# Optimization experiments

Measured on AMD Instinct MI355X. Metric: run time of the kernel, lower is better.

The kernel has to match this reference:

```python
import jax, jax.numpy as jnp
import numpy as np

N_SENT = 65536
N_BAGS = 4096
REL_DIM = 768
FLAT_C = 53
GLOBAL_C = 95


def setup_inputs() -> dict:
    key = jax.random.key(0)
    k1, k2, k3, k4, k5 = jax.random.split(key, 5)
    x = jax.random.normal(k1, (N_SENT, REL_DIM), dtype=jnp.float32)
    attention_query = jax.random.randint(k2, (N_SENT, 3), 0, GLOBAL_C, dtype=jnp.int32)
    # strictly increasing interior boundaries -> every bag non-empty
    rng = np.random.RandomState(0)
    interior = np.sort(rng.choice(np.arange(1, N_SENT), N_BAGS - 1, replace=False))
    scope = jnp.asarray(np.concatenate([[0], interior, [N_SENT]]), dtype=jnp.int32)
    # learned params (xavier-like scale for embeddings, normal bias)
    attention_weight = jax.random.normal(k3, (GLOBAL_C, REL_DIM), dtype=jnp.float32) * (2.0 / (GLOBAL_C + REL_DIM)) ** 0.5
    relation_weight = jax.random.normal(k4, (FLAT_C, REL_DIM * 3), dtype=jnp.float32) * (2.0 / (FLAT_C + REL_DIM * 3)) ** 0.5
    bias = jax.random.normal(k5, (FLAT_C,), dtype=jnp.float32)
    return {"x": x, "attention_query": attention_query, "scope": scope,
            "attention_weight": attention_weight, "relation_weight": relation_weight,
            "bias": bias}


def _segment_ids(scope, n):
    # scope: [B+1] offsets; build per-sentence bag id via boundary scatter + cumsum
    marks = jnp.zeros((n,), dtype=jnp.int32).at[scope[1:-1]].add(1)
    return jnp.cumsum(marks)


def reference(x, attention_query, scope, attention_weight, relation_weight, bias):
    n = x.shape[0]
    n_bags = scope.shape[0] - 1
    seg = _segment_ids(scope, n)  # [N]

    # per-layer attention logits: sum(x * attention_emb, -1) for all 3 layers at once
    att = attention_weight[attention_query]                # [N, 3, D]
    logit = jnp.einsum('nd,nld->nl', x, att)               # [N, 3]

    # segment (per-bag) softmax over sentences, per layer
    seg_max = jax.ops.segment_max(logit, seg, num_segments=n_bags)   # [B, 3]
    w = jnp.exp(logit - seg_max[seg])
    denom = jax.ops.segment_sum(w, seg, num_segments=n_bags)         # [B, 3]
    w = w / denom[seg]                                               # [N, 3]

    # weighted sentence aggregation per bag, per layer
    bag = jax.ops.segment_sum(w[:, :, None] * x[:, None, :], seg, num_segments=n_bags)  # [B, 3, D]

    stack_logits_layers = jnp.transpose(bag, (1, 0, 2))    # [3, B, D]
    logits_total = bag.reshape(n_bags, -1)                 # [B, 3*D] == cat(layer0, layer1, layer2)
    # dropout in eval mode (identity); global_ratio > 0 -> compute probs
    probs = logits_total @ relation_weight.T + bias        # [B, FLAT_C]
    return (stack_logits_layers, logits_total, probs)
```

## Files before the change

### kernel.cpp

```cpp
#include <hip/hip_runtime.h>
#include <math.h>

#define NSENT 65536
#define NBAGS 4096
#define DIM 768
#define D4 192
#define FLATC 53
#define CPAD 64
#define KTOT 2304
#define K4 576
#define CHUNK 256

typedef short bf16x8 __attribute__((ext_vector_type(8)));
typedef float f32x4 __attribute__((ext_vector_type(4)));

__device__ __forceinline__ float wsum(float v) {
#pragma unroll
  for (int o = 32; o; o >>= 1) v += __shfl_xor(v, o);
  return v;
}
__device__ __forceinline__ float wmax(float v) {
#pragma unroll
  for (int o = 32; o; o >>= 1) v = fmaxf(v, __shfl_xor(v, o));
  return v;
}
__device__ __forceinline__ float dot4(float4 a, float4 b) {
  return a.x * b.x + a.y * b.y + a.z * b.z + a.w * b.w;
}
__device__ __forceinline__ unsigned short f2bf(float f) {
  unsigned int u = __float_as_uint(f);
  return (unsigned short)((u + 0x7FFFu + ((u >> 16) & 1u)) >> 16);
}

__global__ __launch_bounds__(192) void bag_kernel(
    const float* __restrict__ x, const int* __restrict__ q,
    const int* __restrict__ scope, const float* __restrict__ aw,
    float* __restrict__ out, unsigned short* __restrict__ lt16) {
  const int b = blockIdx.x;
  const int s0 = scope[b];
  const int s1 = scope[b + 1];
  const int len = s1 - s0;
  const int tid = threadIdx.x;
  const int wave = tid >> 6;
  const int lane = tid & 63;

  __shared__ float lg[CHUNK][3];
  __shared__ int sq[CHUNK][3];
  __shared__ float sm[3], se[3];

  float m[3] = {-INFINITY, -INFINITY, -INFINITY};
  float dsum[3] = {0.f, 0.f, 0.f};
  float4 acc[3];
#pragma unroll
  for (int l = 0; l < 3; l++) acc[l] = make_float4(0.f, 0.f, 0.f, 0.f);

  const float4* __restrict__ X4 = (const float4*)x;
  const float4* __restrict__ AW4 = (const float4*)aw;

  for (int cs = 0; cs < len; cs += CHUNK) {
    const int clen = min(CHUNK, len - cs);

    for (int idx = tid; idx < 3 * clen; idx += 192)
      ((int*)sq)[idx] = q[(size_t)(s0 + cs) * 3 + idx];
    __syncthreads();

    for (int i0 = wave; i0 < clen; i0 += 6) {
      const int i1 = i0 + 3;
      const bool h2 = (i1 < clen);
      const int i1c = h2 ? i1 : i0;
      const int n0 = s0 + cs + i0;
      const int n1 = s0 + cs + i1c;
      const int qa0 = sq[i0][0], qa1 = sq[i0][1], qa2 = sq[i0][2];
      const int qb0 = sq[i1c][0], qb1 = sq[i1c][1], qb2 = sq[i1c][2];
      const float4* xr0 = X4 + (size_t)n0 * D4;
      const float4* xr1 = X4 + (size_t)n1 * D4;
      const float4* A00 = AW4 + (size_t)qa0 * D4;
      const float4* A01 = AW4 + (size_t)qa1 * D4;
      const float4* A02 = AW4 + (size_t)qa2 * D4;
      const float4* A10 = AW4 + (size_t)qb0 * D4;
      const float4* A11 = AW4 + (size_t)qb1 * D4;
      const float4* A12 = AW4 + (size_t)qb2 * D4;
      float p00 = 0.f, p01 = 0.f, p02 = 0.f;
      float p10 = 0.f, p11 = 0.f, p12 = 0.f;
#pragma unroll
      for (int j = 0; j < 3; j++) {
        const int idx = lane + 64 * j;
        const float4 x0 = xr0[idx];
        const float4 x1 = xr1[idx];
        p00 += dot4(x0, A00[idx]);
        p01 += dot4(x0, A01[idx]);
        p02 += dot4(x0, A02[idx]);
        p10 += dot4(x1, A10[idx]);
        p11 += dot4(x1, A11[idx]);
        p12 += dot4(x1, A12[idx]);
      }
      p00 = wsum(p00); p01 = wsum(p01); p02 = wsum(p02);
      p10 = wsum(p10); p11 = wsum(p11); p12 = wsum(p12);
      if (lane == 0) {
        lg[i0][0] = p00; lg[i0][1] = p01; lg[i0][2] = p02;
        if (h2) { lg[i1][0] = p10; lg[i1][1] = p11; lg[i1][2] = p12; }
      }
    }
    __syncthreads();

    {
      const int l = wave;
      float cm = -INFINITY;
      for (int i = lane; i < clen; i += 64) cm = fmaxf(cm, lg[i][l]);
      cm = wmax(cm);
      const float mn = fmaxf(m[l], cm);
      float es = 0.f;
      for (int i = lane; i < clen; i += 64) {
        const float e = __expf(lg[i][l] - mn);
        es += e;
        lg[i][l] = e;
      }
      es = wsum(es);
      if (lane == 0) {
        sm[l] = mn;
        se[l] = es;
      }
    }
    __syncthreads();

#pragma unroll
    for (int l = 0; l < 3; l++) {
      const float mn = sm[l];
      const float sc = __expf(m[l] - mn);
      m[l] = mn;
      dsum[l] = dsum[l] * sc + se[l];
      acc[l].x *= sc; acc[l].y *= sc; acc[l].z *= sc; acc[l].w *= sc;
    }

    {
      int i = 0;
      for (; i + 1 < clen; i += 2) {
        const float w00 = lg[i][0], w01 = lg[i][1], w02 = lg[i][2];
        const float w10 = lg[i + 1][0], w11 = lg[i + 1][1], w12 = lg[i + 1][2];
        const float4 x0 = X4[(size_t)(s0 + cs + i) * D4 + tid];
        const float4 x1 = X4[(size_t)(s0 + cs + i + 1) * D4 + tid];
        acc[0].x += w00 * x0.x + w10 * x1.x;
        acc[0].y += w00 * x0.y + w10 * x1.y;
        acc[0].z += w00 * x0.z + w10 * x1.z;
        acc[0].w += w00 * x0.w + w10 * x1.w;
        acc[1].x += w01 * x0.x + w11 * x1.x;
        acc[1].y += w01 * x0.y + w11 * x1.y;
        acc[1].z += w01 * x0.z + w11 * x1.z;
        acc[1].w += w01 * x0.w + w11 * x1.w;
        acc[2].x += w02 * x0.x + w12 * x1.x;
        acc[2].y += w02 * x0.y + w12 * x1.y;
        acc[2].z += w02 * x0.z + w12 * x1.z;
        acc[2].w += w02 * x0.w + w12 * x1.w;
      }
      if (i < clen) {
        const float w0 = lg[i][0], w1 = lg[i][1], w2 = lg[i][2];
        const float4 xv = X4[(size_t)(s0 + cs + i) * D4 + tid];
        acc[0].x += w0 * xv.x; acc[0].y += w0 * xv.y; acc[0].z += w0 * xv.z; acc[0].w += w0 * xv.w;
        acc[1].x += w1 * xv.x; acc[1].y += w1 * xv.y; acc[1].z += w1 * xv.z; acc[1].w += w1 * xv.w;
        acc[2].x += w2 * xv.x; acc[2].y += w2 * xv.y; acc[2].z += w2 * xv.z; acc[2].w += w2 * xv.w;
      }
    }
    __syncthreads();
  }

  float4* o0 = (float4*)out;
  float4* o1 = (float4*)(out + (size_t)3 * NBAGS * DIM);
  ushort4* l16 = (ushort4*)(lt16 + (size_t)b * KTOT);
#pragma unroll
  for (int l = 0; l < 3; l++) {
    const float inv = (dsum[l] > 0.f) ? (1.f / dsum[l]) : 0.f;
    float4 v = acc[l];
    v.x *= inv; v.y *= inv; v.z *= inv; v.w *= inv;
    o0[((size_t)l * NBAGS + b) * D4 + tid] = v;
    o1[(size_t)b * K4 + l * D4 + tid] = v;
    ushort4 h;
    h.x = f2bf(v.x); h.y = f2bf(v.y); h.z = f2bf(v.z); h.w = f2bf(v.w);
    l16[l * D4 + tid] = h;
  }
}

__global__ __launch_bounds__(256) void rwcvt(const float* __restrict__ rw,
                                             unsigned short* __restrict__ rw16) {
  const int idx = blockIdx.x * 256 + threadIdx.x;
  if (idx < CPAD * KTOT) {
    const int row = idx / KTOT;
    const float v = (row < FLATC) ? rw[idx] : 0.f;
    rw16[idx] = f2bf(v);
  }
}

__global__ __launch_bounds__(256) void probs_mfma(
    const unsigned short* __restrict__ lt16,
    const unsigned short* __restrict__ rw16,
    const float* __restrict__ bias, float* __restrict__ outp) {
  const int wv = threadIdx.x >> 6;
  const int lane = threadIdx.x & 63;
  const int r = lane & 15;
  const int kg = lane >> 4;
  const int bagbase = blockIdx.x * 64 + wv * 16;

  f32x4 acc[4];
#pragma unroll
  for (int ct = 0; ct < 4; ct++) acc[ct] = (f32x4){0.f, 0.f, 0.f, 0.f};

  const unsigned short* ap = lt16 + (size_t)(bagbase + r) * KTOT + kg * 8;
  const unsigned short* bp[4];
#pragma unroll
  for (int ct = 0; ct < 4; ct++)
    bp[ct] = rw16 + (size_t)(ct * 16 + r) * KTOT + kg * 8;

  for (int k = 0; k < KTOT; k += 32) {
    const bf16x8 a = *(const bf16x8*)(ap + k);
#pragma unroll
    for (int ct = 0; ct < 4; ct++) {
      const bf16x8 bb = *(const bf16x8*)(bp[ct] + k);
      acc[ct] = __builtin_amdgcn_mfma_f32_16x16x32_bf16(a, bb, acc[ct], 0, 0, 0);
    }
  }

#pragma unroll
  for (int ct = 0; ct < 4; ct++) {
    const int col = ct * 16 + r;
    if (col < FLATC) {
      const float bv = bias[col];
#pragma unroll
      for (int reg = 0; reg < 4; reg++) {
        const int bag = bagbase + kg * 4 + reg;
        outp[(size_t)bag * FLATC + col] = acc[ct][reg] + bv;
      }
    }
  }
}

extern "C" void kernel_launch(void* const* d_in, const int* in_sizes, int n_in,
                              void* d_out, int out_size, void* d_ws,
                              size_t ws_size, hipStream_t stream) {
  const float* x = (const float*)d_in[0];
  const int* aq = (const int*)d_in[1];
  const int* scope = (const int*)d_in[2];
  const float* aw = (const float*)d_in[3];
  const float* rw = (const float*)d_in[4];
  const float* bias = (const float*)d_in[5];
  float* out = (float*)d_out;

  unsigned short* lt16 = (unsigned short*)d_ws;
  unsigned short* rw16 = lt16 + (size_t)NBAGS * KTOT;

  hipLaunchKernelGGL(bag_kernel, dim3(NBAGS), dim3(192), 0, stream, x, aq,
                     scope, aw, out, lt16);
  hipLaunchKernelGGL(rwcvt, dim3((CPAD * KTOT + 255) / 256), dim3(256), 0,
                     stream, rw, rw16);

  float* probs = out + (size_t)3 * NBAGS * DIM + (size_t)NBAGS * KTOT;
  hipLaunchKernelGGL(probs_mfma, dim3(NBAGS / 64), dim3(256), 0, stream, lt16,
                     rw16, bias, probs);
}
```

Measured before the change: 187.3 us.

## Split logit computation into a separate sentence-parallel kernel before bag aggregation

Moves the per-sentence attention logit dot products out of the per-bag kernel into a standalone kernel that runs two sentences per wave across all sentences, writing logits to a workspace buffer. The bag kernel then only loads precomputed logits, does the segment softmax and the weighted sum. This removes the load imbalance of uneven bag sizes during the logit phase. The trade-off is that x is now read from memory twice, plus an extra launch. The chunk size is doubled and the weighted-sum loop is unrolled by four to put more loads in flight.

```diff
diff --git a/kernel.cpp b/kernel.cpp
--- a/kernel.cpp
+++ b/kernel.cpp
@@ -9,7 +9,7 @@
 #define CPAD 64
 #define KTOT 2304
 #define K4 576
-#define CHUNK 256
+#define CHUNK 512
 
 typedef short bf16x8 __attribute__((ext_vector_type(8)));
 typedef float f32x4 __attribute__((ext_vector_type(4)));
@@ -32,10 +32,59 @@
   return (unsigned short)((u + 0x7FFFu + ((u >> 16) & 1u)) >> 16);
 }
 
-__global__ __launch_bounds__(192) void bag_kernel(
+__global__ __launch_bounds__(256) void logit_kernel(
     const float* __restrict__ x, const int* __restrict__ q,
-    const int* __restrict__ scope, const float* __restrict__ aw,
-    float* __restrict__ out, unsigned short* __restrict__ lt16) {
+    const float* __restrict__ aw, float* __restrict__ lgout) {
+  const int wid = (blockIdx.x * 256 + threadIdx.x) >> 6;
+  const int lane = threadIdx.x & 63;
+  const int n0 = wid * 2;
+  if (n0 >= NSENT) return;
+  const int n1 = n0 + 1;
+
+  const int qa0 = q[3 * n0 + 0], qa1 = q[3 * n0 + 1], qa2 = q[3 * n0 + 2];
+  const int qb0 = q[3 * n1 + 0], qb1 = q[3 * n1 + 1], qb2 = q[3 * n1 + 2];
+
+  const float4* __restrict__ X4 = (const float4*)x;
+  const float4* __restrict__ AW4 = (const float4*)aw;
+  const float4* xr0 = X4 + (size_t)n0 * D4;
+  const float4* xr1 = X4 + (size_t)n1 * D4;
+  const float4* A00 = AW4 + (size_t)qa0 * D4;
+  const float4* A01 = AW4 + (size_t)qa1 * D4;
+  const float4* A02 = AW4 + (size_t)qa2 * D4;
+  const float4* A10 = AW4 + (size_t)qb0 * D4;
+  const float4* A11 = AW4 + (size_t)qb1 * D4;
+  const float4* A12 = AW4 + (size_t)qb2 * D4;
+
+  float p00 = 0.f, p01 = 0.f, p02 = 0.f;
+  float p10 = 0.f, p11 = 0.f, p12 = 0.f;
+#pragma unroll
+  for (int j = 0; j < 3; j++) {
+    const int idx = lane + 64 * j;
+    const float4 x0 = xr0[idx];
+    const float4 x1 = xr1[idx];
+    p00 += dot4(x0, A00[idx]);
+    p01 += dot4(x0, A01[idx]);
+    p02 += dot4(x0, A02[idx]);
+    p10 += dot4(x1, A10[idx]);
+    p11 += dot4(x1, A11[idx]);
+    p12 += dot4(x1, A12[idx]);
+  }
+  p00 = wsum(p00); p01 = wsum(p01); p02 = wsum(p02);
+  p10 = wsum(p10); p11 = wsum(p11); p12 = wsum(p12);
+  if (lane == 0) {
+    lgout[3 * n0 + 0] = p00;
+    lgout[3 * n0 + 1] = p01;
+    lgout[3 * n0 + 2] = p02;
+    lgout[3 * n1 + 0] = p10;
+    lgout[3 * n1 + 1] = p11;
+    lgout[3 * n1 + 2] = p12;
+  }
+}
+
+__global__ __launch_bounds__(192) void bag_sum(
+    const float* __restrict__ x, const float* __restrict__ lgin,
+    const int* __restrict__ scope, float* __restrict__ out,
+    unsigned short* __restrict__ lt16) {
   const int b = blockIdx.x;
   const int s0 = scope[b];
   const int s1 = scope[b + 1];
@@ -45,7 +94,6 @@
   const int lane = tid & 63;
 
   __shared__ float lg[CHUNK][3];
-  __shared__ int sq[CHUNK][3];
   __shared__ float sm[3], se[3];
 
   float m[3] = {-INFINITY, -INFINITY, -INFINITY};
@@ -55,52 +103,12 @@
   for (int l = 0; l < 3; l++) acc[l] = make_float4(0.f, 0.f, 0.f, 0.f);
 
   const float4* __restrict__ X4 = (const float4*)x;
-  const float4* __restrict__ AW4 = (const float4*)aw;
 
   for (int cs = 0; cs < len; cs += CHUNK) {
     const int clen = min(CHUNK, len - cs);
 
     for (int idx = tid; idx < 3 * clen; idx += 192)
-      ((int*)sq)[idx] = q[(size_t)(s0 + cs) * 3 + idx];
-    __syncthreads();
-
-    for (int i0 = wave; i0 < clen; i0 += 6) {
-      const int i1 = i0 + 3;
-      const bool h2 = (i1 < clen);
-      const int i1c = h2 ? i1 : i0;
-      const int n0 = s0 + cs + i0;
-      const int n1 = s0 + cs + i1c;
-      const int qa0 = sq[i0][0], qa1 = sq[i0][1], qa2 = sq[i0][2];
-      const int qb0 = sq[i1c][0], qb1 = sq[i1c][1], qb2 = sq[i1c][2];
-      const float4* xr0 = X4 + (size_t)n0 * D4;
-      const float4* xr1 = X4 + (size_t)n1 * D4;
-      const float4* A00 = AW4 + (size_t)qa0 * D4;
-      const float4* A01 = AW4 + (size_t)qa1 * D4;
-      const float4* A02 = AW4 + (size_t)qa2 * D4;
-      const float4* A10 = AW4 + (size_t)qb0 * D4;
-      const float4* A11 = AW4 + (size_t)qb1 * D4;
-      const float4* A12 = AW4 + (size_t)qb2 * D4;
-      float p00 = 0.f, p01 = 0.f, p02 = 0.f;
-      float p10 = 0.f, p11 = 0.f, p12 = 0.f;
-#pragma unroll
-      for (int j = 0; j < 3; j++) {
-        const int idx = lane + 64 * j;
-        const float4 x0 = xr0[idx];
-        const float4 x1 = xr1[idx];
-        p00 += dot4(x0, A00[idx]);
-        p01 += dot4(x0, A01[idx]);
-        p02 += dot4(x0, A02[idx]);
-        p10 += dot4(x1, A10[idx]);
-        p11 += dot4(x1, A11[idx]);
-        p12 += dot4(x1, A12[idx]);
-      }
-      p00 = wsum(p00); p01 = wsum(p01); p02 = wsum(p02);
-      p10 = wsum(p10); p11 = wsum(p11); p12 = wsum(p12);
-      if (lane == 0) {
-        lg[i0][0] = p00; lg[i0][1] = p01; lg[i0][2] = p02;
-        if (h2) { lg[i1][0] = p10; lg[i1][1] = p11; lg[i1][2] = p12; }
-      }
-    }
+      ((float*)lg)[idx] = lgin[(size_t)(s0 + cs) * 3 + idx];
     __syncthreads();
 
     {
@@ -134,30 +142,32 @@
 
     {
       int i = 0;
-      for (; i + 1 < clen; i += 2) {
-        const float w00 = lg[i][0], w01 = lg[i][1], w02 = lg[i][2];
-        const float w10 = lg[i + 1][0], w11 = lg[i + 1][1], w12 = lg[i + 1][2];
-        const float4 x0 = X4[(size_t)(s0 + cs + i) * D4 + tid];
-        const float4 x1 = X4[(size_t)(s0 + cs + i + 1) * D4 + tid];
-        acc[0].x += w00 * x0.x + w10 * x1.x;
-        acc[0].y += w00 * x0.y + w10 * x1.y;
-        acc[0].z += w00 * x0.z + w10 * x1.z;
-        acc[0].w += w00 * x0.w + w10 * x1.w;
-        acc[1].x += w01 * x0.x + w11 * x1.x;
-        acc[1].y += w01 * x0.y + w11 * x1.y;
-        acc[1].z += w01 * x0.z + w11 * x1.z;
-        acc[1].w += w01 * x0.w + w11 * x1.w;
-        acc[2].x += w02 * x0.x + w12 * x1.x;
-        acc[2].y += w02 * x0.y + w12 * x1.y;
-        acc[2].z += w02 * x0.z + w12 * x1.z;
-        acc[2].w += w02 * x0.w + w12 * x1.w;
-      }
-      if (i < clen) {
-        const float w0 = lg[i][0], w1 = lg[i][1], w2 = lg[i][2];
+      for (; i + 4 <= clen; i += 4) {
+        float4 xv[4];
+        float w0[4], w1[4], w2[4];
+#pragma unroll
+        for (int j = 0; j < 4; j++) {
+          xv[j] = X4[(size_t)(s0 + cs + i + j) * D4 + tid];
+          w0[j] = lg[i + j][0];
+          w1[j] = lg[i + j][1];
+          w2[j] = lg[i + j][2];
+        }
+#pragma unroll
+        for (int j = 0; j < 4; j++) {
+          acc[0].x += w0[j] * xv[j].x; acc[0].y += w0[j] * xv[j].y;
+          acc[0].z += w0[j] * xv[j].z; acc[0].w += w0[j] * xv[j].w;
+          acc[1].x += w1[j] * xv[j].x; acc[1].y += w1[j] * xv[j].y;
+          acc[1].z += w1[j] * xv[j].z; acc[1].w += w1[j] * xv[j].w;
+          acc[2].x += w2[j] * xv[j].x; acc[2].y += w2[j] * xv[j].y;
+          acc[2].z += w2[j] * xv[j].z; acc[2].w += w2[j] * xv[j].w;
+        }
+      }
+      for (; i < clen; i++) {
+        const float a0 = lg[i][0], a1 = lg[i][1], a2 = lg[i][2];
         const float4 xv = X4[(size_t)(s0 + cs + i) * D4 + tid];
-        acc[0].x += w0 * xv.x; acc[0].y += w0 * xv.y; acc[0].z += w0 * xv.z; acc[0].w += w0 * xv.w;
-        acc[1].x += w1 * xv.x; acc[1].y += w1 * xv.y; acc[1].z += w1 * xv.z; acc[1].w += w1 * xv.w;
-        acc[2].x += w2 * xv.x; acc[2].y += w2 * xv.y; acc[2].z += w2 * xv.z; acc[2].w += w2 * xv.w;
+        acc[0].x += a0 * xv.x; acc[0].y += a0 * xv.y; acc[0].z += a0 * xv.z; acc[0].w += a0 * xv.w;
+        acc[1].x += a1 * xv.x; acc[1].y += a1 * xv.y; acc[1].z += a1 * xv.z; acc[1].w += a1 * xv.w;
+        acc[2].x += a2 * xv.x; acc[2].y += a2 * xv.y; acc[2].z += a2 * xv.z; acc[2].w += a2 * xv.w;
       }
     }
     __syncthreads();
@@ -245,9 +255,12 @@
 
   unsigned short* lt16 = (unsigned short*)d_ws;
   unsigned short* rw16 = lt16 + (size_t)NBAGS * KTOT;
-
-  hipLaunchKernelGGL(bag_kernel, dim3(NBAGS), dim3(192), 0, stream, x, aq,
-                     scope, aw, out, lt16);
+  float* lgbuf = (float*)(rw16 + (size_t)CPAD * KTOT);
+
+  hipLaunchKernelGGL(logit_kernel, dim3(NSENT / 2 / 4), dim3(256), 0, stream,
+                     x, aq, aw, lgbuf);
+  hipLaunchKernelGGL(bag_sum, dim3(NBAGS), dim3(192), 0, stream, x, lgbuf,
+                     scope, out, lt16);
   hipLaunchKernelGGL(rwcvt, dim3((CPAD * KTOT + 255) / 256), dim3(256), 0,
                      stream, rw, rw16);
 
```

Measured after the change: 162.0 us. 13.5% less time.

## Stage sentence chunk in LDS as bf16 to read x once per bag

Applied to the files above, without the earlier changes.

Loads each chunk of 16 sentence rows from global memory once, converts to bf16 and keeps them in shared memory. Both the attention-logit dot products and the weighted aggregation then read from LDS, instead of reading x from global memory twice. This reduces global traffic but reduces precision of logits and bag outputs to bf16 inputs. The smaller chunk also adds more barriers per bag.

```diff
diff --git a/kernel.cpp b/kernel.cpp
--- a/kernel.cpp
+++ b/kernel.cpp
@@ -1,4 +1,5 @@
 #include <hip/hip_runtime.h>
+#include <hip/hip_bf16.h>
 #include <math.h>
 
 #define NSENT 65536
@@ -9,7 +10,7 @@
 #define CPAD 64
 #define KTOT 2304
 #define K4 576
-#define CHUNK 256
+#define CH 16
 
 typedef short bf16x8 __attribute__((ext_vector_type(8)));
 typedef float f32x4 __attribute__((ext_vector_type(4)));
@@ -28,13 +29,34 @@
   return a.x * b.x + a.y * b.y + a.z * b.z + a.w * b.w;
 }
 __device__ __forceinline__ unsigned short f2bf(float f) {
-  unsigned int u = __float_as_uint(f);
-  return (unsigned short)((u + 0x7FFFu + ((u >> 16) & 1u)) >> 16);
-}
-
-__global__ __launch_bounds__(192) void bag_kernel(
+  union { __hip_bfloat16 b; unsigned short s; } cv;
+  cv.b = __float2bfloat16(f);
+  return cv.s;
+}
+__device__ __forceinline__ float bf2f(unsigned short s) {
+  return __uint_as_float(((unsigned int)s) << 16);
+}
+__device__ __forceinline__ ushort4 pk4(float4 v) {
+  ushort4 h;
+  h.x = f2bf(v.x); h.y = f2bf(v.y); h.z = f2bf(v.z); h.w = f2bf(v.w);
+  return h;
+}
+__device__ __forceinline__ float4 up4(ushort4 h) {
+  return make_float4(bf2f(h.x), bf2f(h.y), bf2f(h.z), bf2f(h.w));
+}
+
+__global__ __launch_bounds__(256) void rwcvt(const float* __restrict__ rw,
+                                             unsigned short* __restrict__ rw16) {
+  const int idx = blockIdx.x * 256 + threadIdx.x;
+  if (idx < CPAD * KTOT) {
+    const int row = idx / KTOT;
+    rw16[idx] = f2bf(row < FLATC ? rw[idx] : 0.f);
+  }
+}
+
+__global__ __launch_bounds__(192) void fused_bag(
     const float* __restrict__ x, const int* __restrict__ q,
-    const int* __restrict__ scope, const float* __restrict__ aw,
+    const float* __restrict__ aw, const int* __restrict__ scope,
     float* __restrict__ out, unsigned short* __restrict__ lt16) {
   const int b = blockIdx.x;
   const int s0 = scope[b];
@@ -44,8 +66,8 @@
   const int wave = tid >> 6;
   const int lane = tid & 63;
 
-  __shared__ float lg[CHUNK][3];
-  __shared__ int sq[CHUNK][3];
+  __shared__ ushort4 xs[CH * D4];
+  __shared__ float lg[CH][3];
   __shared__ float sm[3], se[3];
 
   float m[3] = {-INFINITY, -INFINITY, -INFINITY};
@@ -57,49 +79,45 @@
   const float4* __restrict__ X4 = (const float4*)x;
   const float4* __restrict__ AW4 = (const float4*)aw;
 
-  for (int cs = 0; cs < len; cs += CHUNK) {
-    const int clen = min(CHUNK, len - cs);
-
-    for (int idx = tid; idx < 3 * clen; idx += 192)
-      ((int*)sq)[idx] = q[(size_t)(s0 + cs) * 3 + idx];
-    __syncthreads();
-
-    for (int i0 = wave; i0 < clen; i0 += 6) {
-      const int i1 = i0 + 3;
-      const bool h2 = (i1 < clen);
-      const int i1c = h2 ? i1 : i0;
-      const int n0 = s0 + cs + i0;
-      const int n1 = s0 + cs + i1c;
-      const int qa0 = sq[i0][0], qa1 = sq[i0][1], qa2 = sq[i0][2];
-      const int qb0 = sq[i1c][0], qb1 = sq[i1c][1], qb2 = sq[i1c][2];
-      const float4* xr0 = X4 + (size_t)n0 * D4;
-      const float4* xr1 = X4 + (size_t)n1 * D4;
-      const float4* A00 = AW4 + (size_t)qa0 * D4;
-      const float4* A01 = AW4 + (size_t)qa1 * D4;
-      const float4* A02 = AW4 + (size_t)qa2 * D4;
-      const float4* A10 = AW4 + (size_t)qb0 * D4;
-      const float4* A11 = AW4 + (size_t)qb1 * D4;
-      const float4* A12 = AW4 + (size_t)qb2 * D4;
-      float p00 = 0.f, p01 = 0.f, p02 = 0.f;
-      float p10 = 0.f, p11 = 0.f, p12 = 0.f;
+  for (int cs = 0; cs < len; cs += CH) {
+    const int clen = min(CH, len - cs);
+
+    {
+      int i = 0;
+      for (; i + 4 <= clen; i += 4) {
+        float4 v0 = X4[(size_t)(s0 + cs + i + 0) * D4 + tid];
+        float4 v1 = X4[(size_t)(s0 + cs + i + 1) * D4 + tid];
+        float4 v2 = X4[(size_t)(s0 + cs + i + 2) * D4 + tid];
+        float4 v3 = X4[(size_t)(s0 + cs + i + 3) * D4 + tid];
+        xs[(i + 0) * D4 + tid] = pk4(v0);
+        xs[(i + 1) * D4 + tid] = pk4(v1);
+        xs[(i + 2) * D4 + tid] = pk4(v2);
+        xs[(i + 3) * D4 + tid] = pk4(v3);
+      }
+      for (; i < clen; i++)
+        xs[i * D4 + tid] = pk4(X4[(size_t)(s0 + cs + i) * D4 + tid]);
+    }
+    __syncthreads();
+
+    for (int i = wave; i < clen; i += 3) {
+      const int n = s0 + cs + i;
+      const int q0 = q[3 * n + 0];
+      const int q1 = q[3 * n + 1];
+      const int q2 = q[3 * n + 2];
+      const float4* A0 = AW4 + (size_t)q0 * D4;
+      const float4* A1 = AW4 + (size_t)q1 * D4;
+      const float4* A2 = AW4 + (size_t)q2 * D4;
+      float p0 = 0.f, p1 = 0.f, p2 = 0.f;
 #pragma unroll
       for (int j = 0; j < 3; j++) {
-        const int idx = lane + 64 * j;
-        const float4 x0 = xr0[idx];
-        const float4 x1 = xr1[idx];
-        p00 += dot4(x0, A00[idx]);
-        p01 += dot4(x0, A01[idx]);
-        p02 += dot4(x0, A02[idx]);
-        p10 += dot4(x1, A10[idx]);
-        p11 += dot4(x1, A11[idx]);
-        p12 += dot4(x1, A12[idx]);
-      }
-      p00 = wsum(p00); p01 = wsum(p01); p02 = wsum(p02);
-      p10 = wsum(p10); p11 = wsum(p11); p12 = wsum(p12);
-      if (lane == 0) {
-        lg[i0][0] = p00; lg[i0][1] = p01; lg[i0][2] = p02;
-        if (h2) { lg[i1][0] = p10; lg[i1][1] = p11; lg[i1][2] = p12; }
-      }
+        const int c = lane + 64 * j;
+        const float4 xv = up4(xs[i * D4 + c]);
+        p0 += dot4(xv, A0[c]);
+        p1 += dot4(xv, A1[c]);
+        p2 += dot4(xv, A2[c]);
+      }
+      p0 = wsum(p0); p1 = wsum(p1); p2 = wsum(p2);
+      if (lane == 0) { lg[i][0] = p0; lg[i][1] = p1; lg[i][2] = p2; }
     }
     __syncthreads();
 
@@ -116,10 +134,7 @@
         lg[i][l] = e;
       }
       es = wsum(es);
-      if (lane == 0) {
-        sm[l] = mn;
-        se[l] = es;
-      }
+      if (lane == 0) { sm[l] = mn; se[l] = es; }
     }
     __syncthreads();
 
@@ -134,11 +149,11 @@
 
     {
       int i = 0;
-      for (; i + 1 < clen; i += 2) {
+      for (; i + 2 <= clen; i += 2) {
         const float w00 = lg[i][0], w01 = lg[i][1], w02 = lg[i][2];
         const float w10 = lg[i + 1][0], w11 = lg[i + 1][1], w12 = lg[i + 1][2];
-        const float4 x0 = X4[(size_t)(s0 + cs + i) * D4 + tid];
-        const float4 x1 = X4[(size_t)(s0 + cs + i + 1) * D4 + tid];
+        const float4 x0 = up4(xs[i * D4 + tid]);
+        const float4 x1 = up4(xs[(i + 1) * D4 + tid]);
         acc[0].x += w00 * x0.x + w10 * x1.x;
         acc[0].y += w00 * x0.y + w10 * x1.y;
         acc[0].z += w00 * x0.z + w10 * x1.z;
@@ -153,11 +168,11 @@
         acc[2].w += w02 * x0.w + w12 * x1.w;
       }
       if (i < clen) {
-        const float w0 = lg[i][0], w1 = lg[i][1], w2 = lg[i][2];
-        const float4 xv = X4[(size_t)(s0 + cs + i) * D4 + tid];
-        acc[0].x += w0 * xv.x; acc[0].y += w0 * xv.y; acc[0].z += w0 * xv.z; acc[0].w += w0 * xv.w;
-        acc[1].x += w1 * xv.x; acc[1].y += w1 * xv.y; acc[1].z += w1 * xv.z; acc[1].w += w1 * xv.w;
-        acc[2].x += w2 * xv.x; acc[2].y += w2 * xv.y; acc[2].z += w2 * xv.z; acc[2].w += w2 * xv.w;
+        const float a0 = lg[i][0], a1 = lg[i][1], a2 = lg[i][2];
+        const float4 xv = up4(xs[i * D4 + tid]);
+        acc[0].x += a0 * xv.x; acc[0].y += a0 * xv.y; acc[0].z += a0 * xv.z; acc[0].w += a0 * xv.w;
+        acc[1].x += a1 * xv.x; acc[1].y += a1 * xv.y; acc[1].z += a1 * xv.z; acc[1].w += a1 * xv.w;
+        acc[2].x += a2 * xv.x; acc[2].y += a2 * xv.y; acc[2].z += a2 * xv.z; acc[2].w += a2 * xv.w;
       }
     }
     __syncthreads();
@@ -173,19 +188,7 @@
     v.x *= inv; v.y *= inv; v.z *= inv; v.w *= inv;
     o0[((size_t)l * NBAGS + b) * D4 + tid] = v;
     o1[(size_t)b * K4 + l * D4 + tid] = v;
-    ushort4 h;
-    h.x = f2bf(v.x); h.y = f2bf(v.y); h.z = f2bf(v.z); h.w = f2bf(v.w);
-    l16[l * D4 + tid] = h;
-  }
-}
-
-__global__ __launch_bounds__(256) void rwcvt(const float* __restrict__ rw,
-                                             unsigned short* __restrict__ rw16) {
-  const int idx = blockIdx.x * 256 + threadIdx.x;
-  if (idx < CPAD * KTOT) {
-    const int row = idx / KTOT;
-    const float v = (row < FLATC) ? rw[idx] : 0.f;
-    rw16[idx] = f2bf(v);
+    l16[l * D4 + tid] = pk4(v);
   }
 }
 
@@ -246,10 +249,10 @@
   unsigned short* lt16 = (unsigned short*)d_ws;
   unsigned short* rw16 = lt16 + (size_t)NBAGS * KTOT;
 
-  hipLaunchKernelGGL(bag_kernel, dim3(NBAGS), dim3(192), 0, stream, x, aq,
-                     scope, aw, out, lt16);
   hipLaunchKernelGGL(rwcvt, dim3((CPAD * KTOT + 255) / 256), dim3(256), 0,
                      stream, rw, rw16);
+  hipLaunchKernelGGL(fused_bag, dim3(NBAGS), dim3(192), 0, stream, x, aq, aw,
+                     scope, out, lt16);
 
   float* probs = out + (size_t)3 * NBAGS * DIM + (size_t)NBAGS * KTOT;
   hipLaunchKernelGGL(probs_mfma, dim3(NBAGS / 64), dim3(256), 0, stream, lt16,
```

Measured after the change: 194.7 us. 3.9% more time.

## Process eight bags per block with one wave per bag for softmax aggregation

Applied to the files above, without the earlier changes.

Replaces the one-bag-per-block kernel with a 512-thread block covering eight consecutive bags. All waves compute attention logits cooperatively over the combined sentence span, then each wave runs the online softmax and weighted sum for its own bag, recomputing the exponentials inline. The aim is to fix the load imbalance and poor utilisation of tiny bags (about 16 sentences each), and to drop the shared staging of query indices. The cost is more registers per thread, since nine float4 accumulators are held per lane. Each bag is now reduced by a single wave instead of three, which limits parallelism within a bag.

```diff
diff --git a/kernel.cpp b/kernel.cpp
--- a/kernel.cpp
+++ b/kernel.cpp
@@ -1,4 +1,5 @@
 #include <hip/hip_runtime.h>
+#include <hip/hip_bf16.h>
 #include <math.h>
 
 #define NSENT 65536
@@ -9,7 +10,9 @@
 #define CPAD 64
 #define KTOT 2304
 #define K4 576
-#define CHUNK 256
+#define GB 8
+#define NW 8
+#define CHF 256
 
 typedef short bf16x8 __attribute__((ext_vector_type(8)));
 typedef float f32x4 __attribute__((ext_vector_type(4)));
@@ -28,52 +31,69 @@
   return a.x * b.x + a.y * b.y + a.z * b.z + a.w * b.w;
 }
 __device__ __forceinline__ unsigned short f2bf(float f) {
-  unsigned int u = __float_as_uint(f);
-  return (unsigned short)((u + 0x7FFFu + ((u >> 16) & 1u)) >> 16);
-}
-
-__global__ __launch_bounds__(192) void bag_kernel(
+  union { __hip_bfloat16 b; unsigned short s; } cv;
+  cv.b = __float2bfloat16(f);
+  return cv.s;
+}
+__device__ __forceinline__ ushort4 pk4(float4 v) {
+  ushort4 h;
+  h.x = f2bf(v.x); h.y = f2bf(v.y); h.z = f2bf(v.z); h.w = f2bf(v.w);
+  return h;
+}
+
+__global__ __launch_bounds__(256) void rwcvt(const float* __restrict__ rw,
+                                             unsigned short* __restrict__ rw16) {
+  const int idx = blockIdx.x * 256 + threadIdx.x;
+  if (idx < CPAD * KTOT) {
+    const int row = idx / KTOT;
+    rw16[idx] = f2bf(row < FLATC ? rw[idx] : 0.f);
+  }
+}
+
+__global__ __launch_bounds__(512) void fused8(
     const float* __restrict__ x, const int* __restrict__ q,
-    const int* __restrict__ scope, const float* __restrict__ aw,
+    const float* __restrict__ aw, const int* __restrict__ scope,
     float* __restrict__ out, unsigned short* __restrict__ lt16) {
-  const int b = blockIdx.x;
-  const int s0 = scope[b];
-  const int s1 = scope[b + 1];
-  const int len = s1 - s0;
   const int tid = threadIdx.x;
-  const int wave = tid >> 6;
+  const int wv = tid >> 6;
   const int lane = tid & 63;
-
-  __shared__ float lg[CHUNK][3];
-  __shared__ int sq[CHUNK][3];
-  __shared__ float sm[3], se[3];
-
-  float m[3] = {-INFINITY, -INFINITY, -INFINITY};
-  float dsum[3] = {0.f, 0.f, 0.f};
-  float4 acc[3];
-#pragma unroll
-  for (int l = 0; l < 3; l++) acc[l] = make_float4(0.f, 0.f, 0.f, 0.f);
+  const int b0 = blockIdx.x * GB;
+
+  __shared__ int sscope[GB + 1];
+  __shared__ float lg[CHF][3];
+
+  if (tid <= GB) sscope[tid] = scope[b0 + tid];
+  __syncthreads();
+  const int n0 = sscope[0];
+  const int span = sscope[GB] - n0;
 
   const float4* __restrict__ X4 = (const float4*)x;
   const float4* __restrict__ AW4 = (const float4*)aw;
 
-  for (int cs = 0; cs < len; cs += CHUNK) {
-    const int clen = min(CHUNK, len - cs);
-
-    for (int idx = tid; idx < 3 * clen; idx += 192)
-      ((int*)sq)[idx] = q[(size_t)(s0 + cs) * 3 + idx];
-    __syncthreads();
-
-    for (int i0 = wave; i0 < clen; i0 += 6) {
-      const int i1 = i0 + 3;
+  float m0 = -INFINITY, m1 = -INFINITY, m2 = -INFINITY;
+  float d0 = 0.f, d1 = 0.f, d2 = 0.f;
+  float4 acc[3][3];
+#pragma unroll
+  for (int l = 0; l < 3; l++)
+#pragma unroll
+    for (int k = 0; k < 3; k++) acc[l][k] = make_float4(0.f, 0.f, 0.f, 0.f);
+
+  const int bss = sscope[wv] - n0;
+  const int bee = sscope[wv + 1] - n0;
+
+  for (int cs = 0; cs < span; cs += CHF) {
+    const int clen = min(CHF, span - cs);
+
+    for (int i0 = wv; i0 < clen; i0 += 2 * NW) {
+      const int i1 = i0 + NW;
       const bool h2 = (i1 < clen);
       const int i1c = h2 ? i1 : i0;
-      const int n0 = s0 + cs + i0;
-      const int n1 = s0 + cs + i1c;
-      const int qa0 = sq[i0][0], qa1 = sq[i0][1], qa2 = sq[i0][2];
-      const int qb0 = sq[i1c][0], qb1 = sq[i1c][1], qb2 = sq[i1c][2];
-      const float4* xr0 = X4 + (size_t)n0 * D4;
-      const float4* xr1 = X4 + (size_t)n1 * D4;
+      const int na = n0 + cs + i0;
+      const int nb = n0 + cs + i1c;
+      const int qa0 = q[3 * na + 0], qa1 = q[3 * na + 1], qa2 = q[3 * na + 2];
+      const int qb0 = q[3 * nb + 0], qb1 = q[3 * nb + 1], qb2 = q[3 * nb + 2];
+      const float4* xr0 = X4 + (size_t)na * D4;
+      const float4* xr1 = X4 + (size_t)nb * D4;
       const float4* A00 = AW4 + (size_t)qa0 * D4;
       const float4* A01 = AW4 + (size_t)qa1 * D4;
       const float4* A02 = AW4 + (size_t)qa2 * D4;
@@ -84,15 +104,15 @@
       float p10 = 0.f, p11 = 0.f, p12 = 0.f;
 #pragma unroll
       for (int j = 0; j < 3; j++) {
-        const int idx = lane + 64 * j;
-        const float4 x0 = xr0[idx];
-        const float4 x1 = xr1[idx];
-        p00 += dot4(x0, A00[idx]);
-        p01 += dot4(x0, A01[idx]);
-        p02 += dot4(x0, A02[idx]);
-        p10 += dot4(x1, A10[idx]);
-        p11 += dot4(x1, A11[idx]);
-        p12 += dot4(x1, A12[idx]);
+        const int c = lane + 64 * j;
+        const float4 x0 = xr0[c];
+        const float4 x1 = xr1[c];
+        p00 += dot4(x0, A00[c]);
+        p01 += dot4(x0, A01[c]);
+        p02 += dot4(x0, A02[c]);
+        p10 += dot4(x1, A10[c]);
+        p11 += dot4(x1, A11[c]);
+        p12 += dot4(x1, A12[c]);
       }
       p00 = wsum(p00); p01 = wsum(p01); p02 = wsum(p02);
       p10 = wsum(p10); p11 = wsum(p11); p12 = wsum(p12);
@@ -104,88 +124,99 @@
     __syncthreads();
 
     {
-      const int l = wave;
-      float cm = -INFINITY;
-      for (int i = lane; i < clen; i += 64) cm = fmaxf(cm, lg[i][l]);
-      cm = wmax(cm);
-      const float mn = fmaxf(m[l], cm);
-      float es = 0.f;
-      for (int i = lane; i < clen; i += 64) {
-        const float e = __expf(lg[i][l] - mn);
-        es += e;
-        lg[i][l] = e;
-      }
-      es = wsum(es);
-      if (lane == 0) {
-        sm[l] = mn;
-        se[l] = es;
+      const int ss = max(bss - cs, 0);
+      const int ee = min(bee - cs, clen);
+      if (ss < ee) {
+        float c0 = -INFINITY, c1 = -INFINITY, c2 = -INFINITY;
+        for (int i = ss + lane; i < ee; i += 64) {
+          c0 = fmaxf(c0, lg[i][0]);
+          c1 = fmaxf(c1, lg[i][1]);
+          c2 = fmaxf(c2, lg[i][2]);
+        }
+        c0 = wmax(c0); c1 = wmax(c1); c2 = wmax(c2);
+        const float n0m = fmaxf(m0, c0);
+        const float n1m = fmaxf(m1, c1);
+        const float n2m = fmaxf(m2, c2);
+        const float s0 = __expf(m0 - n0m);
+        const float s1 = __expf(m1 - n1m);
+        const float s2 = __expf(m2 - n2m);
+        m0 = n0m; m1 = n1m; m2 = n2m;
+        d0 *= s0; d1 *= s1; d2 *= s2;
+#pragma unroll
+        for (int k = 0; k < 3; k++) {
+          acc[0][k].x *= s0; acc[0][k].y *= s0; acc[0][k].z *= s0; acc[0][k].w *= s0;
+          acc[1][k].x *= s1; acc[1][k].y *= s1; acc[1][k].z *= s1; acc[1][k].w *= s1;
+          acc[2][k].x *= s2; acc[2][k].y *= s2; acc[2][k].z *= s2; acc[2][k].w *= s2;
+        }
+        int i = ss;
+        for (; i + 2 <= ee; i += 2) {
+          const int na = n0 + cs + i;
+          const int nb = na + 1;
+          const float wa0 = __expf(lg[i][0] - m0);
+          const float wa1 = __expf(lg[i][1] - m1);
+          const float wa2 = __expf(lg[i][2] - m2);
+          const float wb0 = __expf(lg[i + 1][0] - m0);
+          const float wb1 = __expf(lg[i + 1][1] - m1);
+          const float wb2 = __expf(lg[i + 1][2] - m2);
+          d0 += wa0 + wb0; d1 += wa1 + wb1; d2 += wa2 + wb2;
+#pragma unroll
+          for (int k = 0; k < 3; k++) {
+            const float4 xa = X4[(size_t)na * D4 + lane + 64 * k];
+            const float4 xb = X4[(size_t)nb * D4 + lane + 64 * k];
+            acc[0][k].x += wa0 * xa.x + wb0 * xb.x;
+            acc[0][k].y += wa0 * xa.y + wb0 * xb.y;
+            acc[0][k].z += wa0 * xa.z + wb0 * xb.z;
+            acc[0][k].w += wa0 * xa.w + wb0 * xb.w;
+            acc[1][k].x += wa1 * xa.x + wb1 * xb.x;
+            acc[1][k].y += wa1 * xa.y + wb1 * xb.y;
+            acc[1][k].z += wa1 * xa.z + wb1 * xb.z;
+            acc[1][k].w += wa1 * xa.w + wb1 * xb.w;
+            acc[2][k].x += wa2 * xa.x + wb2 * xb.x;
+            acc[2][k].y += wa2 * xa.y + wb2 * xb.y;
+            acc[2][k].z += wa2 * xa.z + wb2 * xb.z;
+            acc[2][k].w += wa2 * xa.w + wb2 * xb.w;
+          }
+        }
+        if (i < ee) {
+          const int na = n0 + cs + i;
+          const float wa0 = __expf(lg[i][0] - m0);
+          const float wa1 = __expf(lg[i][1] - m1);
+          const float wa2 = __expf(lg[i][2] - m2);
+          d0 += wa0; d1 += wa1; d2 += wa2;
+#pragma unroll
+          for (int k = 0; k < 3; k++) {
+            const float4 xa = X4[(size_t)na * D4 + lane + 64 * k];
+            acc[0][k].x += wa0 * xa.x; acc[0][k].y += wa0 * xa.y;
+            acc[0][k].z += wa0 * xa.z; acc[0][k].w += wa0 * xa.w;
+            acc[1][k].x += wa1 * xa.x; acc[1][k].y += wa1 * xa.y;
+            acc[1][k].z += wa1 * xa.z; acc[1][k].w += wa1 * xa.w;
+            acc[2][k].x += wa2 * xa.x; acc[2][k].y += wa2 * xa.y;
+            acc[2][k].z += wa2 * xa.z; acc[2][k].w += wa2 * xa.w;
+          }
+        }
       }
     }
     __syncthreads();
-
-#pragma unroll
-    for (int l = 0; l < 3; l++) {
-      const float mn = sm[l];
-      const float sc = __expf(m[l] - mn);
-      m[l] = mn;
-      dsum[l] = dsum[l] * sc + se[l];
-      acc[l].x *= sc; acc[l].y *= sc; acc[l].z *= sc; acc[l].w *= sc;
-    }
-
-    {
-      int i = 0;
-      for (; i + 1 < clen; i += 2) {
-        const float w00 = lg[i][0], w01 = lg[i][1], w02 = lg[i][2];
-        const float w10 = lg[i + 1][0], w11 = lg[i + 1][1], w12 = lg[i + 1][2];
-        const float4 x0 = X4[(size_t)(s0 + cs + i) * D4 + tid];
-        const float4 x1 = X4[(size_t)(s0 + cs + i + 1) * D4 + tid];
-        acc[0].x += w00 * x0.x + w10 * x1.x;
-        acc[0].y += w00 * x0.y + w10 * x1.y;
-        acc[0].z += w00 * x0.z + w10 * x1.z;
-        acc[0].w += w00 * x0.w + w10 * x1.w;
-        acc[1].x += w01 * x0.x + w11 * x1.x;
-        acc[1].y += w01 * x0.y + w11 * x1.y;
-        acc[1].z += w01 * x0.z + w11 * x1.z;
-        acc[1].w += w01 * x0.w + w11 * x1.w;
-        acc[2].x += w02 * x0.x + w12 * x1.x;
-        acc[2].y += w02 * x0.y + w12 * x1.y;
-        acc[2].z += w02 * x0.z + w12 * x1.z;
-        acc[2].w += w02 * x0.w + w12 * x1.w;
-      }
-      if (i < clen) {
-        const float w0 = lg[i][0], w1 = lg[i][1], w2 = lg[i][2];
-        const float4 xv = X4[(size_t)(s0 + cs + i) * D4 + tid];
-        acc[0].x += w0 * xv.x; acc[0].y += w0 * xv.y; acc[0].z += w0 * xv.z; acc[0].w += w0 * xv.w;
-        acc[1].x += w1 * xv.x; acc[1].y += w1 * xv.y; acc[1].z += w1 * xv.z; acc[1].w += w1 * xv.w;
-        acc[2].x += w2 * xv.x; acc[2].y += w2 * xv.y; acc[2].z += w2 * xv.z; acc[2].w += w2 * xv.w;
-      }
-    }
-    __syncthreads();
-  }
-
+  }
+
+  const int b = b0 + wv;
   float4* o0 = (float4*)out;
   float4* o1 = (float4*)(out + (size_t)3 * NBAGS * DIM);
   ushort4* l16 = (ushort4*)(lt16 + (size_t)b * KTOT);
+  const float di[3] = {(d0 > 0.f) ? 1.f / d0 : 0.f,
+                       (d1 > 0.f) ? 1.f / d1 : 0.f,
+                       (d2 > 0.f) ? 1.f / d2 : 0.f};
 #pragma unroll
   for (int l = 0; l < 3; l++) {
-    const float inv = (dsum[l] > 0.f) ? (1.f / dsum[l]) : 0.f;
-    float4 v = acc[l];
-    v.x *= inv; v.y *= inv; v.z *= inv; v.w *= inv;
-    o0[((size_t)l * NBAGS + b) * D4 + tid] = v;
-    o1[(size_t)b * K4 + l * D4 + tid] = v;
-    ushort4 h;
-    h.x = f2bf(v.x); h.y = f2bf(v.y); h.z = f2bf(v.z); h.w = f2bf(v.w);
-    l16[l * D4 + tid] = h;
-  }
-}
-
-__global__ __launch_bounds__(256) void rwcvt(const float* __restrict__ rw,
-                                             unsigned short* __restrict__ rw16) {
-  const int idx = blockIdx.x * 256 + threadIdx.x;
-  if (idx < CPAD * KTOT) {
-    const int row = idx / KTOT;
-    const float v = (row < FLATC) ? rw[idx] : 0.f;
-    rw16[idx] = f2bf(v);
+#pragma unroll
+    for (int k = 0; k < 3; k++) {
+      const int c = lane + 64 * k;
+      float4 v = acc[l][k];
+      v.x *= di[l]; v.y *= di[l]; v.z *= di[l]; v.w *= di[l];
+      o0[((size_t)l * NBAGS + b) * D4 + c] = v;
+      o1[(size_t)b * K4 + l * D4 + c] = v;
+      l16[l * D4 + c] = pk4(v);
+    }
   }
 }
 
@@ -246,10 +277,10 @@
   unsigned short* lt16 = (unsigned short*)d_ws;
   unsigned short* rw16 = lt16 + (size_t)NBAGS * KTOT;
 
-  hipLaunchKernelGGL(bag_kernel, dim3(NBAGS), dim3(192), 0, stream, x, aq,
-                     scope, aw, out, lt16);
   hipLaunchKernelGGL(rwcvt, dim3((CPAD * KTOT + 255) / 256), dim3(256), 0,
                      stream, rw, rw16);
+  hipLaunchKernelGGL(fused8, dim3(NBAGS / GB), dim3(512), 0, stream, x, aq,
+                     aw, scope, out, lt16);
 
   float* probs = out + (size_t)3 * NBAGS * DIM + (size_t)NBAGS * KTOT;
   hipLaunchKernelGGL(probs_mfma, dim3(NBAGS / 64), dim3(256), 0, stream, lt16,
```

Result: slower. 197.2 us (+5.3%).
